# Performance work log

Hardware: AMD Instinct MI355X
Metric: run time of the kernel (lower is better)

## Reference

```python
import jax, jax.numpy as jnp
import numpy as np

D_K = 64
N_STEPS = 4
NEG = -1e9  # stand-in for -inf; keeps vjp NaN-free, numerically identical softmax


def setup_inputs() -> dict:
    key = jax.random.key(0)
    ks = jax.random.split(key, 12)
    B, N, D = 4, 2048, 1024
    s = 0.02
    return {
        "hidden": jax.random.normal(ks[0], (B, N, D), jnp.float32),
        "W1": jax.random.normal(ks[1], (64, D), jnp.float32) * s,
        "b1": jnp.zeros((64,), jnp.float32),
        "W2": jax.random.normal(ks[2], (28, 64), jnp.float32) * s,
        "b2": jnp.zeros((28,), jnp.float32),
        "Wq": jax.random.normal(ks[3], (D_K, 28), jnp.float32) * s,
        "Wk": jax.random.normal(ks[4], (D_K, 28), jnp.float32) * s,
        "Wc": jax.random.normal(ks[5], (1, 28), jnp.float32) * s,
        "bc": jnp.zeros((1,), jnp.float32),
        "Wv": jax.random.normal(ks[6], (D_K, D), jnp.float32) * s,
        "Wo": jax.random.normal(ks[7], (D, D_K), jnp.float32) * s,  # torch inits this to zeros; randomized for a non-trivial baseline
        "step_size": jnp.asarray(0.5, jnp.float32),
        "charge_decay": jnp.asarray(0.3, jnp.float32),
        "layer_idx": 0,
    }


def reference(hidden, W1, b1, W2, b2, Wq, Wk, Wc, bc, Wv, Wo, step_size, charge_decay, layer_idx):
    B, N, D = hidden.shape
    # features come from detached hidden in the torch code
    h_sg = jax.lax.stop_gradient(hidden)
    f = jax.nn.gelu(h_sg @ W1.T + b1, approximate=False)  # [B,N,64]
    features = jax.nn.sigmoid(f @ W2.T + b2)              # [B,N,28]
    Q = features @ Wq.T                                   # [B,N,64]
    K = features @ Wk.T                                   # [B,N,64]
    compat = jnp.einsum('bnd,bmd->bnm', Q, K) / jnp.float32(np.sqrt(D_K))
    charge = jax.nn.sigmoid(features @ Wc.T + bc)[..., 0]  # [B,N]
    causal = jnp.tril(jnp.ones((N, N), dtype=bool))
    logits = jnp.where(causal, compat, NEG)
    for _ in range(N_STEPS):
        attn = jax.nn.softmax(logits, axis=-1)            # [B,N,N]
        received = attn.sum(axis=-2)                      # [B,N]
        charge = charge * (1.0 - charge_decay * jax.nn.sigmoid(received - 1.0))
        energy = -compat * charge[:, :, None] * charge[:, None, :]
        logits = jnp.where(causal, logits - step_size * energy, NEG)
    attn = jax.nn.softmax(logits, axis=-1)
    V = hidden @ Wv.T                                     # [B,N,64]
    out = jnp.einsum('bnm,bmd->bnd', attn, V) @ Wo.T      # [B,N,D]
    return out * 0.1
```

## Files before the change

kernel.cpp:

```cpp
#include <hip/hip_runtime.h>
#include <hip/hip_bf16.h>

typedef unsigned short ushort_t;
typedef short bf16x8 __attribute__((ext_vector_type(8)));
typedef ushort_t u16x8 __attribute__((ext_vector_type(8)));
typedef ushort_t u16x4 __attribute__((ext_vector_type(4)));
typedef float f32x4 __attribute__((ext_vector_type(4)));

#define DEV static __device__ __forceinline__

DEV float bf2f(ushort_t u) { unsigned v = ((unsigned)u) << 16; float f; __builtin_memcpy(&f, &v, 4); return f; }
DEV short f2bf(float x) { __hip_bfloat16 h = __float2bfloat16(x); short s; __builtin_memcpy(&s, &h, 2); return s; }
DEV float sigm(float x) { return 1.0f / (1.0f + __expf(-x)); }

DEV bf16x8 cvt8(float4 a0, float4 a1) {
    bf16x8 t;
    t[0] = f2bf(a0.x); t[1] = f2bf(a0.y); t[2] = f2bf(a0.z); t[3] = f2bf(a0.w);
    t[4] = f2bf(a1.x); t[5] = f2bf(a1.y); t[6] = f2bf(a1.z); t[7] = f2bf(a1.w);
    return t;
}
DEV bf16x8 ld8f(const float* __restrict__ p) {
    return cvt8(*reinterpret_cast<const float4*>(p), *reinterpret_cast<const float4*>(p + 4));
}

__global__ void k_cvtW(const float* __restrict__ W1, const float* __restrict__ Wv,
                       ushort_t* __restrict__ Wcat) {
    int i = blockIdx.x * 256 + threadIdx.x;
    const float* src = (i < 8192) ? (W1 + (long)i * 8) : (Wv + (long)(i - 8192) * 8);
    const float4* p = reinterpret_cast<const float4*>(src);
    *reinterpret_cast<bf16x8*>(Wcat + (long)i * 8) = cvt8(p[0], p[1]);
}

__global__ __launch_bounds__(256) void k_fvfeat(const float* __restrict__ hidden,
        const ushort_t* __restrict__ Wcat, const float* __restrict__ b1,
        const float* __restrict__ W2, const float* __restrict__ b2,
        const float* __restrict__ Wq, const float* __restrict__ Wk,
        const float* __restrict__ Wc, const float* __restrict__ bc,
        ushort_t* __restrict__ Qb, ushort_t* __restrict__ Kb,
        ushort_t* __restrict__ VbT, float* __restrict__ charge0) {
    __shared__ float w2L[28 * 65], wqL[64 * 29], wkL[64 * 29], wcL[28], b2L[28];
    __shared__ float fLDS[16][65], featL[4][28];
    int tid = threadIdx.x;
    for (int i = tid; i < 28 * 64; i += 256) w2L[(i >> 6) * 65 + (i & 63)] = W2[i];
    for (int i = tid; i < 64 * 28; i += 256) {
        int r = i / 28, c = i - r * 28;
        wqL[r * 29 + c] = Wq[i];
        wkL[r * 29 + c] = Wk[i];
    }
    if (tid < 28) { wcL[tid] = Wc[tid]; b2L[tid] = b2[tid]; }

    int m0 = blockIdx.x * 16;
    int wave = tid >> 6, lane = tid & 63, l16 = lane & 15, quad = lane >> 4;
    int cb = (wave & 1) * 32;
    int brow_off = (wave < 2) ? 0 : 64;
    f32x4 acc[2] = {};
    const float* arow = hidden + (long)(m0 + l16) * 1024;
    const ushort_t* brow0 = Wcat + (long)(brow_off + cb + l16) * 1024;
    const ushort_t* brow1 = Wcat + (long)(brow_off + cb + 16 + l16) * 1024;
    for (int kc = 0; kc < 1024; kc += 128) {
#pragma unroll
        for (int u = 0; u < 4; u++) {
            int ko = kc + u * 32 + quad * 8;
            bf16x8 a = ld8f(arow + ko);
            bf16x8 b0 = *reinterpret_cast<const bf16x8*>(brow0 + ko);
            bf16x8 b1f = *reinterpret_cast<const bf16x8*>(brow1 + ko);
            acc[0] = __builtin_amdgcn_mfma_f32_16x16x32_bf16(a, b0, acc[0], 0, 0, 0);
            acc[1] = __builtin_amdgcn_mfma_f32_16x16x32_bf16(a, b1f, acc[1], 0, 0, 0);
        }
    }
    if (wave < 2) {
        float b1a = b1[cb + l16], b1b = b1[cb + 16 + l16];
#pragma unroll
        for (int c = 0; c < 2; c++) {
            float bv = c ? b1b : b1a;
#pragma unroll
            for (int rr = 0; rr < 4; rr++) {
                float x = acc[c][rr] + bv;
                fLDS[quad * 4 + rr][cb + c * 16 + l16] =
                    0.5f * x * (1.0f + erff(x * 0.70710678118654752f));
            }
        }
    } else {
#pragma unroll
        for (int c = 0; c < 2; c++)
#pragma unroll
            for (int rr = 0; rr < 4; rr++)
                VbT[(long)(cb + c * 16 + l16) * 8192 + (m0 + quad * 4 + rr)] =
                    (ushort_t)f2bf(acc[c][rr]);
    }
    __syncthreads();
    float bcv = bc[0];
    for (int it = 0; it < 4; it++) {
        int rowl = it * 4 + wave;
        int row = m0 + rowl;
        if (lane < 28) {
            float s = b2L[lane];
#pragma unroll
            for (int j = 0; j < 64; j++) s += fLDS[rowl][j] * w2L[lane * 65 + j];
            featL[wave][lane] = sigm(s);
        }
        __syncthreads();
        float q = 0.f, k = 0.f;
#pragma unroll
        for (int i = 0; i < 28; i++) {
            float fv = featL[wave][i];
            q += fv * wqL[lane * 29 + i];
            k += fv * wkL[lane * 29 + i];
        }
        Qb[row * 64 + lane] = (ushort_t)f2bf(q * 0.125f);
        Kb[row * 64 + lane] = (ushort_t)f2bf(k);
        if (lane == 0) {
            float c = bcv;
#pragma unroll
            for (int i = 0; i < 28; i++) c += featL[wave][i] * wcL[i];
            charge0[row] = sigm(c);
        }
        __syncthreads();
    }
}

DEV void tri_decode(int r, int& ti, int& tj) {
    int t = (int)((sqrtf(8.f * (float)r + 1.f) - 1.f) * 0.5f);
    while ((t + 1) * (t + 2) / 2 <= r) t++;
    while (t * (t + 1) / 2 > r) t--;
    ti = t;
    tj = r - t * (t + 1) / 2;
}

__global__ __launch_bounds__(256) void k_compat(const ushort_t* __restrict__ Qb,
                                                const ushort_t* __restrict__ Kb,
                                                ushort_t* __restrict__ compat) {
    int bid = blockIdx.x;
    int b = bid / 136, r = bid % 136, ti, tj;
    tri_decode(r, ti, tj);
    int wave = threadIdx.x >> 6, lane = threadIdx.x & 63;
    int l16 = lane & 15, quad = lane >> 4;
    int rbase = b * 2048 + ti * 128 + wave * 32;
    int cbase = b * 2048 + tj * 128;
    f32x4 acc[2][8] = {};
#pragma unroll
    for (int kc = 0; kc < 64; kc += 32) {
        int ko = kc + quad * 8;
        bf16x8 af[2], bf[8];
#pragma unroll
        for (int f = 0; f < 2; f++)
            af[f] = *reinterpret_cast<const bf16x8*>(Qb + (long)(rbase + f * 16 + l16) * 64 + ko);
#pragma unroll
        for (int f = 0; f < 8; f++)
            bf[f] = *reinterpret_cast<const bf16x8*>(Kb + (long)(cbase + f * 16 + l16) * 64 + ko);
#pragma unroll
        for (int i = 0; i < 2; i++)
#pragma unroll
            for (int j = 0; j < 8; j++)
                acc[i][j] = __builtin_amdgcn_mfma_f32_16x16x32_bf16(af[i], bf[j], acc[i][j], 0, 0, 0);
    }
    int colt = tj * 128;
#pragma unroll
    for (int i = 0; i < 2; i++)
#pragma unroll
        for (int j = 0; j < 8; j++)
#pragma unroll
            for (int rr = 0; rr < 4; rr++) {
                long rowg = rbase + i * 16 + quad * 4 + rr;
                int col = colt + j * 16 + l16;
                compat[rowg * 2048 + col] = (ushort_t)f2bf(acc[i][j][rr]);
            }
}

template <int T>
__global__ __launch_bounds__(256, 2) void k_strip(const ushort_t* __restrict__ compat,
        const float4* __restrict__ charges4, const float* __restrict__ stepp,
        float* __restrict__ Rpart) {
    __shared__ float chR[4][8];
    __shared__ float red[4][8], Li[8];
    int bid = blockIdx.x, tid = threadIdx.x;
    int b = bid >> 8, pi = bid & 255;
    int r0A = pi * 4, r0B = 2044 - pi * 4;
    float step = stepp[0];
    if (T > 0 && tid < 8) {
        int row = (tid < 4) ? (r0A + tid) : (r0B + tid - 4);
        float4 c4 = charges4[b * 2048 + row];
        chR[0][tid] = step * c4.x;
        if (T > 1) chR[1][tid] = step * c4.y;
        if (T > 2) chR[2][tid] = step * c4.z;
        if (T > 3) chR[3][tid] = step * c4.w;
    }
    __syncthreads();
    int w = tid >> 6, lane = tid & 63;
    int c0 = tid * 4;
    const ushort_t* base = compat + (long)(b * 2048) * 2048;

    float pA[4][4] = {}, pB0[4][4] = {}, pB1[4][4] = {};
    float SA[4] = {}, SB[4] = {};

    {
        float cx[4] = {}, cy[4] = {}, cz[4] = {}, cw[4] = {};
        if (T > 0) {
#pragma unroll
            for (int k = 0; k < 4; k++) {
                float4 c = charges4[b * 2048 + c0 + k];
                cx[k] = c.x;
                if (T > 1) cy[k] = c.y;
                if (T > 2) cz[k] = c.z;
                if (T > 3) cw[k] = c.w;
            }
        }
        if (c0 <= r0A + 3) {
#pragma unroll
            for (int rr = 0; rr < 4; rr++) {
                u16x4 v = *reinterpret_cast<const u16x4*>(base + (long)(r0A + rr) * 2048 + c0);
#pragma unroll
                for (int k = 0; k < 4; k++) {
                    float sg = 1.f;
                    if (T > 0) sg += chR[0][rr] * cx[k];
                    if (T > 1) sg += chR[1][rr] * cy[k];
                    if (T > 2) sg += chR[2][rr] * cz[k];
                    if (T > 3) sg += chR[3][rr] * cw[k];
                    float p = (c0 + k <= r0A + rr) ? __expf(bf2f(v[k]) * sg) : 0.f;
                    pA[rr][k] = p;
                    SA[rr] += p;
                }
            }
        }
#pragma unroll
        for (int rr = 0; rr < 4; rr++) {
            u16x4 v = *reinterpret_cast<const u16x4*>(base + (long)(r0B + rr) * 2048 + c0);
#pragma unroll
            for (int k = 0; k < 4; k++) {
                float sg = 1.f;
                if (T > 0) sg += chR[0][4 + rr] * cx[k];
                if (T > 1) sg += chR[1][4 + rr] * cy[k];
                if (T > 2) sg += chR[2][4 + rr] * cz[k];
                if (T > 3) sg += chR[3][4 + rr] * cw[k];
                float p = __expf(bf2f(v[k]) * sg);
                pB0[rr][k] = p;
                SB[rr] += p;
            }
        }
    }
    if (1024 + c0 <= r0B + 3) {
        float cx[4] = {}, cy[4] = {}, cz[4] = {}, cw[4] = {};
        if (T > 0) {
#pragma unroll
            for (int k = 0; k < 4; k++) {
                float4 c = charges4[b * 2048 + 1024 + c0 + k];
                cx[k] = c.x;
                if (T > 1) cy[k] = c.y;
                if (T > 2) cz[k] = c.z;
                if (T > 3) cw[k] = c.w;
            }
        }
#pragma unroll
        for (int rr = 0; rr < 4; rr++) {
            u16x4 v = *reinterpret_cast<const u16x4*>(base + (long)(r0B + rr) * 2048 + 1024 + c0);
#pragma unroll
            for (int k = 0; k < 4; k++) {
                float sg = 1.f;
                if (T > 0) sg += chR[0][4 + rr] * cx[k];
                if (T > 1) sg += chR[1][4 + rr] * cy[k];
                if (T > 2) sg += chR[2][4 + rr] * cz[k];
                if (T > 3) sg += chR[3][4 + rr] * cw[k];
                float p = (1024 + c0 + k <= r0B + rr) ? __expf(bf2f(v[k]) * sg) : 0.f;
                pB1[rr][k] = p;
                SB[rr] += p;
            }
        }
    }
#pragma unroll
    for (int rr = 0; rr < 4; rr++) {
        float s = SA[rr];
        s += __shfl_xor(s, 1); s += __shfl_xor(s, 2); s += __shfl_xor(s, 4);
        s += __shfl_xor(s, 8); s += __shfl_xor(s, 16); s += __shfl_xor(s, 32);
        if (lane == 0) red[w][rr] = s;
        float t = SB[rr];
        t += __shfl_xor(t, 1); t += __shfl_xor(t, 2); t += __shfl_xor(t, 4);
        t += __shfl_xor(t, 8); t += __shfl_xor(t, 16); t += __shfl_xor(t, 32);
        if (lane == 0) red[w][4 + rr] = t;
    }
    __syncthreads();
    if (tid < 8) Li[tid] = 1.f / fmaxf(red[0][tid] + red[1][tid] + red[2][tid] + red[3][tid], 1e-30f);
    __syncthreads();
    float liA0 = Li[0], liA1 = Li[1], liA2 = Li[2], liA3 = Li[3];
    float liB0 = Li[4], liB1 = Li[5], liB2 = Li[6], liB3 = Li[7];
    float4 o0, o1;
    float* po0 = (float*)&o0;
    float* po1 = (float*)&o1;
#pragma unroll
    for (int k = 0; k < 4; k++) {
        po0[k] = pA[0][k] * liA0 + pA[1][k] * liA1 + pA[2][k] * liA2 + pA[3][k] * liA3
               + pB0[0][k] * liB0 + pB0[1][k] * liB1 + pB0[2][k] * liB2 + pB0[3][k] * liB3;
        po1[k] = pB1[0][k] * liB0 + pB1[1][k] * liB1 + pB1[2][k] * liB2 + pB1[3][k] * liB3;
    }
    *reinterpret_cast<float4*>(&Rpart[(long)bid * 2048 + c0]) = o0;
    *reinterpret_cast<float4*>(&Rpart[(long)bid * 2048 + 1024 + c0]) = o1;
}

template <int T>
__global__ __launch_bounds__(256) void k_charge(const float* __restrict__ Rpart,
        const float* __restrict__ charge0, float4* __restrict__ charges4,
        const float* __restrict__ decayp) {
    __shared__ float s8[8][33];
    int g = threadIdx.x >> 5, cl = threadIdx.x & 31;
    int m = blockIdx.x * 32 + cl;
    int b = m >> 11, col = m & 2047;
    const float* rp = Rpart + ((long)(b * 256 + g * 32) * 2048) + col;
    float s = 0.f;
#pragma unroll
    for (int i = 0; i < 32; i++) s += rp[(long)i * 2048];
    s8[g][cl] = s;
    __syncthreads();
    if (threadIdx.x < 32) {
        float t = 0.f;
#pragma unroll
        for (int gg = 0; gg < 8; gg++) t += s8[gg][threadIdx.x];
        int mm = blockIdx.x * 32 + threadIdx.x;
        float decay = decayp[0];
        float prev = (T == 1) ? charge0[mm] : ((const float*)&charges4[mm])[T - 2];
        ((float*)&charges4[mm])[T - 1] = prev * (1.f - decay * sigm(t - 1.f));
    }
}

__global__ __launch_bounds__(256, 4) void k_stripPV(const ushort_t* __restrict__ compat,
        const float4* __restrict__ charges4, const float* __restrict__ stepp,
        const ushort_t* __restrict__ VbT, ushort_t* __restrict__ Abf) {
    __shared__ float chR[4][8], red[4][8], Li[8];
    __shared__ __align__(16) ushort_t pbuf[9][1032];
    int bid = blockIdx.x, tid = threadIdx.x;
    int b = bid >> 8, pi = bid & 255;
    int r0A = pi * 4, r0B = 2044 - pi * 4;
    float step = stepp[0];
    if (tid < 8) {
        int row = (tid < 4) ? (r0A + tid) : (r0B + tid - 4);
        float4 c4 = charges4[b * 2048 + row];
        chR[0][tid] = step * c4.x; chR[1][tid] = step * c4.y;
        chR[2][tid] = step * c4.z; chR[3][tid] = step * c4.w;
    }
    u16x4 zz = {0, 0, 0, 0};
    *reinterpret_cast<u16x4*>(&pbuf[8][tid * 4]) = zz;
    __syncthreads();
    int w = tid >> 6, lane = tid & 63, l16 = lane & 15, quad = lane >> 4;
    int pr = (l16 < 8) ? l16 : 8;
    int c0 = tid * 4;
    const ushort_t* base = compat + (long)(b * 2048) * 2048;
    float S[8];
#pragma unroll
    for (int i = 0; i < 8; i++) S[i] = 0.f;
    f32x4 acc = {};

    {
        float cx[4], cy[4], cz[4], cw[4];
#pragma unroll
        for (int k = 0; k < 4; k++) {
            float4 c = charges4[b * 2048 + c0 + k];
            cx[k] = c.x; cy[k] = c.y; cz[k] = c.z; cw[k] = c.w;
        }
        if (c0 <= r0A + 3) {
#pragma unroll
            for (int i = 0; i < 4; i++) {
                u16x4 v = *reinterpret_cast<const u16x4*>(base + (long)(r0A + i) * 2048 + c0);
                u16x4 pv;
#pragma unroll
                for (int k = 0; k < 4; k++) {
                    float sg = 1.f + chR[0][i] * cx[k] + chR[1][i] * cy[k]
                                   + chR[2][i] * cz[k] + chR[3][i] * cw[k];
                    float p = (c0 + k <= r0A + i) ? __expf(bf2f(v[k]) * sg) : 0.f;
                    S[i] += p;
                    pv[k] = (ushort_t)f2bf(p);
                }
                *reinterpret_cast<u16x4*>(&pbuf[i][c0]) = pv;
            }
        } else {
#pragma unroll
            for (int i = 0; i < 4; i++) *reinterpret_cast<u16x4*>(&pbuf[i][c0]) = zz;
        }
#pragma unroll
        for (int i = 4; i < 8; i++) {
            u16x4 v = *reinterpret_cast<const u16x4*>(base + (long)(r0B + i - 4) * 2048 + c0);
            u16x4 pv;
#pragma unroll
            for (int k = 0; k < 4; k++) {
                float sg = 1.f + chR[0][i] * cx[k] + chR[1][i] * cy[k]
                               + chR[2][i] * cz[k] + chR[3][i] * cw[k];
                float p = __expf(bf2f(v[k]) * sg);
                S[i] += p;
                pv[k] = (ushort_t)f2bf(p);
            }
            *reinterpret_cast<u16x4*>(&pbuf[i][c0]) = pv;
        }
    }
    __syncthreads();
#pragma unroll 4
    for (int k0 = 0; k0 < 1024; k0 += 32) {
        bf16x8 af = *reinterpret_cast<const bf16x8*>(&pbuf[pr][k0 + quad * 8]);
        bf16x8 vf = *reinterpret_cast<const bf16x8*>(
            VbT + (long)(w * 16 + l16) * 8192 + b * 2048 + k0 + quad * 8);
        acc = __builtin_amdgcn_mfma_f32_16x16x32_bf16(af, vf, acc, 0, 0, 0);
    }
    __syncthreads();
    {
#pragma unroll
        for (int i = 0; i < 4; i++) *reinterpret_cast<u16x4*>(&pbuf[i][c0]) = zz;
        if (1024 + c0 <= r0B + 3) {
            float cx[4], cy[4], cz[4], cw[4];
#pragma unroll
            for (int k = 0; k < 4; k++) {
                float4 c = charges4[b * 2048 + 1024 + c0 + k];
                cx[k] = c.x; cy[k] = c.y; cz[k] = c.z; cw[k] = c.w;
            }
#pragma unroll
            for (int i = 4; i < 8; i++) {
                int grow = r0B + i - 4;
                u16x4 v = *reinterpret_cast<const u16x4*>(base + (long)grow * 2048 + 1024 + c0);
                u16x4 pv;
#pragma unroll
                for (int k = 0; k < 4; k++) {
                    float sg = 1.f + chR[0][i] * cx[k] + chR[1][i] * cy[k]
                                   + chR[2][i] * cz[k] + chR[3][i] * cw[k];
                    float p = (1024 + c0 + k <= grow) ? __expf(bf2f(v[k]) * sg) : 0.f;
                    S[i] += p;
                    pv[k] = (ushort_t)f2bf(p);
                }
                *reinterpret_cast<u16x4*>(&pbuf[i][c0]) = pv;
            }
        } else {
#pragma unroll
            for (int i = 4; i < 8; i++) *reinterpret_cast<u16x4*>(&pbuf[i][c0]) = zz;
        }
    }
    __syncthreads();
#pragma unroll 4
    for (int k0 = 0; k0 < 1024; k0 += 32) {
        bf16x8 af = *reinterpret_cast<const bf16x8*>(&pbuf[pr][k0 + quad * 8]);
        bf16x8 vf = *reinterpret_cast<const bf16x8*>(
            VbT + (long)(w * 16 + l16) * 8192 + b * 2048 + 1024 + k0 + quad * 8);
        acc = __builtin_amdgcn_mfma_f32_16x16x32_bf16(af, vf, acc, 0, 0, 0);
    }
#pragma unroll
    for (int i = 0; i < 8; i++) {
        float s = S[i];
        s += __shfl_xor(s, 1); s += __shfl_xor(s, 2); s += __shfl_xor(s, 4);
        s += __shfl_xor(s, 8); s += __shfl_xor(s, 16); s += __shfl_xor(s, 32);
        if (lane == 0) red[w][i] = s;
    }
    __syncthreads();
    if (tid < 8) Li[tid] = 1.f / fmaxf(red[0][tid] + red[1][tid] + red[2][tid] + red[3][tid], 1e-30f);
    __syncthreads();
    if (quad < 2) {
#pragma unroll
        for (int rr = 0; rr < 4; rr++) {
            int row8 = quad * 4 + rr;
            int grow = (row8 < 4) ? (b * 2048 + r0A + row8) : (b * 2048 + r0B + row8 - 4);
            Abf[(long)grow * 64 + w * 16 + l16] = (ushort_t)f2bf(acc[rr] * Li[row8]);
        }
    }
}

__global__ __launch_bounds__(256) void k_oproj(const ushort_t* __restrict__ Abf,
                                               const float* __restrict__ Wo,
                                               float* __restrict__ out) {
    int mt = blockIdx.x & 63, nt = blockIdx.x >> 6;
    int wave = threadIdx.x >> 6, lane = threadIdx.x & 63;
    int wm = wave >> 1, wn = wave & 1;
    int l16 = lane & 15, quad = lane >> 4;
    int row0 = mt * 128 + wm * 64;
    int col0 = nt * 128 + wn * 64;
    f32x4 acc[4][4] = {};
#pragma unroll
    for (int kc = 0; kc < 64; kc += 32) {
        int ko = kc + quad * 8;
        bf16x8 af[4], bfm[4];
#pragma unroll
        for (int f = 0; f < 4; f++)
            af[f] = *reinterpret_cast<const bf16x8*>(Abf + (long)(row0 + f * 16 + l16) * 64 + ko);
#pragma unroll
        for (int f = 0; f < 4; f++) bfm[f] = ld8f(Wo + (long)(col0 + f * 16 + l16) * 64 + ko);
#pragma unroll
        for (int i = 0; i < 4; i++)
#pragma unroll
            for (int j = 0; j < 4; j++)
                acc[i][j] = __builtin_amdgcn_mfma_f32_16x16x32_bf16(af[i], bfm[j], acc[i][j], 0, 0, 0);
    }
#pragma unroll
    for (int i = 0; i < 4; i++)
#pragma unroll
        for (int j = 0; j < 4; j++)
#pragma unroll
            for (int rr = 0; rr < 4; rr++) {
                long rowg = row0 + i * 16 + quad * 4 + rr;
                int colg = col0 + j * 16 + l16;
                out[rowg * 1024 + colg] = acc[i][j][rr] * 0.1f;
            }
}

extern "C" void kernel_launch(void* const* d_in, const int* in_sizes, int n_in,
                              void* d_out, int out_size, void* d_ws, size_t ws_size,
                              hipStream_t stream) {
    const float* hidden = (const float*)d_in[0];
    const float* W1 = (const float*)d_in[1];
    const float* b1 = (const float*)d_in[2];
    const float* W2 = (const float*)d_in[3];
    const float* b2 = (const float*)d_in[4];
    const float* Wq = (const float*)d_in[5];
    const float* Wk = (const float*)d_in[6];
    const float* Wc = (const float*)d_in[7];
    const float* bc = (const float*)d_in[8];
    const float* Wv = (const float*)d_in[9];
    const float* Wo = (const float*)d_in[10];
    const float* stepp = (const float*)d_in[11];
    const float* decayp = (const float*)d_in[12];

    char* ws = (char*)d_ws;
    size_t off = 0;
    auto alloc = [&](size_t bytes) {
        void* p = ws + off;
        off += (bytes + 255) & ~(size_t)255;
        return p;
    };
    ushort_t* compat = (ushort_t*)alloc(8192UL * 2048 * 2);
    ushort_t* Wcat = (ushort_t*)alloc(128UL * 1024 * 2);
    ushort_t* Qb = (ushort_t*)alloc(8192UL * 64 * 2);
    ushort_t* Kb = (ushort_t*)alloc(8192UL * 64 * 2);
    ushort_t* VbT = (ushort_t*)alloc(64UL * 8192 * 2);
    float* charge0 = (float*)alloc(8192UL * 4);
    float4* charges4 = (float4*)alloc(8192UL * 16);
    float* Rpart = (float*)alloc(1024UL * 2048 * 4);
    ushort_t* Abf = (ushort_t*)alloc(8192UL * 64 * 2);
    (void)ws_size; (void)in_sizes; (void)n_in; (void)out_size;

    k_cvtW<<<64, 256, 0, stream>>>(W1, Wv, Wcat);
    k_fvfeat<<<512, 256, 0, stream>>>(hidden, Wcat, b1, W2, b2, Wq, Wk, Wc, bc,
                                      Qb, Kb, VbT, charge0);
    k_compat<<<544, 256, 0, stream>>>(Qb, Kb, compat);

    k_strip<0><<<1024, 256, 0, stream>>>(compat, charges4, stepp, Rpart);
    k_charge<1><<<256, 256, 0, stream>>>(Rpart, charge0, charges4, decayp);
    k_strip<1><<<1024, 256, 0, stream>>>(compat, charges4, stepp, Rpart);
    k_charge<2><<<256, 256, 0, stream>>>(Rpart, charge0, charges4, decayp);
    k_strip<2><<<1024, 256, 0, stream>>>(compat, charges4, stepp, Rpart);
    k_charge<3><<<256, 256, 0, stream>>>(Rpart, charge0, charges4, decayp);
    k_strip<3><<<1024, 256, 0, stream>>>(compat, charges4, stepp, Rpart);
    k_charge<4><<<256, 256, 0, stream>>>(Rpart, charge0, charges4, decayp);

    k_stripPV<<<1024, 256, 0, stream>>>(compat, charges4, stepp, VbT, Abf);
    k_oproj<<<512, 256, 0, stream>>>(Abf, Wo, (float*)d_out);
}
```

Before: 261.7 us.

## Stage hidden tile in LDS as bf16 and split K across waves

The feature/V projection kernel now loads each block's 16x1024 hidden tile once with coalesced float4 reads, converts it to bf16 into shared memory, and has the four waves split the K dimension in halves, each computing four output tiles. Partial sums are reduced through a shared buffer before the GELU and V-transpose stores. Previously every wave re-read and re-converted the fp32 hidden row from global memory. In exchange the kernel uses roughly 50KB more LDS per block, which may lower occupancy, and adds an extra barrier and reduction pass.

```diff
diff --git a/kernel.cpp b/kernel.cpp
--- a/kernel.cpp
+++ b/kernel.cpp
@@ -40,7 +40,10 @@
         ushort_t* __restrict__ VbT, float* __restrict__ charge0) {
     __shared__ float w2L[28 * 65], wqL[64 * 29], wkL[64 * 29], wcL[28], b2L[28];
     __shared__ float fLDS[16][65], featL[4][28];
+    __shared__ __align__(16) ushort_t hLDS[16][1032];
+    __shared__ float part[2][8][16][16];
     int tid = threadIdx.x;
+    int m0 = blockIdx.x * 16;
     for (int i = tid; i < 28 * 64; i += 256) w2L[(i >> 6) * 65 + (i & 63)] = W2[i];
     for (int i = tid; i < 64 * 28; i += 256) {
         int r = i / 28, c = i - r * 28;
@@ -48,45 +51,63 @@
         wkL[r * 29 + c] = Wk[i];
     }
     if (tid < 28) { wcL[tid] = Wc[tid]; b2L[tid] = b2[tid]; }
-
-    int m0 = blockIdx.x * 16;
+    {
+        const float4* hp = reinterpret_cast<const float4*>(hidden + (long)m0 * 1024);
+#pragma unroll 4
+        for (int it = 0; it < 16; it++) {
+            int f = it * 256 + tid;
+            int row = f >> 8, colf = f & 255;
+            float4 v = hp[f];
+            u16x4 o;
+            o[0] = (ushort_t)f2bf(v.x); o[1] = (ushort_t)f2bf(v.y);
+            o[2] = (ushort_t)f2bf(v.z); o[3] = (ushort_t)f2bf(v.w);
+            *reinterpret_cast<u16x4*>(&hLDS[row][colf * 4]) = o;
+        }
+    }
+    __syncthreads();
     int wave = tid >> 6, lane = tid & 63, l16 = lane & 15, quad = lane >> 4;
-    int cb = (wave & 1) * 32;
-    int brow_off = (wave < 2) ? 0 : 64;
-    f32x4 acc[2] = {};
-    const float* arow = hidden + (long)(m0 + l16) * 1024;
-    const ushort_t* brow0 = Wcat + (long)(brow_off + cb + l16) * 1024;
-    const ushort_t* brow1 = Wcat + (long)(brow_off + cb + 16 + l16) * 1024;
-    for (int kc = 0; kc < 1024; kc += 128) {
-#pragma unroll
-        for (int u = 0; u < 4; u++) {
-            int ko = kc + u * 32 + quad * 8;
-            bf16x8 a = ld8f(arow + ko);
-            bf16x8 b0 = *reinterpret_cast<const bf16x8*>(brow0 + ko);
-            bf16x8 b1f = *reinterpret_cast<const bf16x8*>(brow1 + ko);
-            acc[0] = __builtin_amdgcn_mfma_f32_16x16x32_bf16(a, b0, acc[0], 0, 0, 0);
-            acc[1] = __builtin_amdgcn_mfma_f32_16x16x32_bf16(a, b1f, acc[1], 0, 0, 0);
-        }
-    }
-    if (wave < 2) {
-        float b1a = b1[cb + l16], b1b = b1[cb + 16 + l16];
-#pragma unroll
-        for (int c = 0; c < 2; c++) {
-            float bv = c ? b1b : b1a;
-#pragma unroll
-            for (int rr = 0; rr < 4; rr++) {
-                float x = acc[c][rr] + bv;
-                fLDS[quad * 4 + rr][cb + c * 16 + l16] =
-                    0.5f * x * (1.0f + erff(x * 0.70710678118654752f));
-            }
-        }
-    } else {
-#pragma unroll
-        for (int c = 0; c < 2; c++)
-#pragma unroll
-            for (int rr = 0; rr < 4; rr++)
-                VbT[(long)(cb + c * 16 + l16) * 8192 + (m0 + quad * 4 + rr)] =
-                    (ushort_t)f2bf(acc[c][rr]);
+    int khalf = wave >> 1, tg = wave & 1;
+    f32x4 acc[4] = {};
+    const ushort_t* bbase = Wcat + (long)(tg * 64 + l16) * 1024;
+    {
+        int kbase = khalf * 512;
+#pragma unroll 2
+        for (int s = 0; s < 16; s++) {
+            int ko = kbase + s * 32 + quad * 8;
+            bf16x8 a = *reinterpret_cast<const bf16x8*>(&hLDS[l16][ko]);
+#pragma unroll
+            for (int i = 0; i < 4; i++) {
+                bf16x8 bfr = *reinterpret_cast<const bf16x8*>(bbase + (long)i * 16384 + ko);
+                acc[i] = __builtin_amdgcn_mfma_f32_16x16x32_bf16(a, bfr, acc[i], 0, 0, 0);
+            }
+        }
+    }
+#pragma unroll
+    for (int i = 0; i < 4; i++)
+#pragma unroll
+        for (int rr = 0; rr < 4; rr++)
+            part[khalf][tg * 4 + i][quad * 4 + rr][l16] = acc[i][rr];
+    __syncthreads();
+    {
+        int t = tid >> 5, r = (tid >> 1) & 15, ch = tid & 1;
+        const float4 a0 = *reinterpret_cast<const float4*>(&part[0][t][r][ch * 8]);
+        const float4 a1 = *reinterpret_cast<const float4*>(&part[0][t][r][ch * 8 + 4]);
+        const float4 c0v = *reinterpret_cast<const float4*>(&part[1][t][r][ch * 8]);
+        const float4 c1v = *reinterpret_cast<const float4*>(&part[1][t][r][ch * 8 + 4]);
+        float v[8] = {a0.x + c0v.x, a0.y + c0v.y, a0.z + c0v.z, a0.w + c0v.w,
+                      a1.x + c1v.x, a1.y + c1v.y, a1.z + c1v.z, a1.w + c1v.w};
+        int colbase = t * 16 + ch * 8;
+        if (t < 4) {
+#pragma unroll
+            for (int j = 0; j < 8; j++) {
+                float x = v[j] + b1[colbase + j];
+                fLDS[r][colbase + j] = 0.5f * x * (1.0f + erff(x * 0.70710678118654752f));
+            }
+        } else {
+#pragma unroll
+            for (int j = 0; j < 8; j++)
+                VbT[(long)(colbase + j - 64) * 8192 + m0 + r] = (ushort_t)f2bf(v[j]);
+        }
     }
     __syncthreads();
     float bcv = bc[0];
```

After: 254.8 us. 2.6% less time.
